# Performance work log

Measured on AMD Instinct MI355X. Metric: run time of the kernel, lower is better.

Reference implementation:

```python
import jax, jax.numpy as jnp
import numpy as np

B, H, W, T, D = 8, 32, 32, 4, 768
BLK = 4  # super-block of base tokens used to generate the static partition


def _build_descs():
    """Deterministic partition: 4x4 blocks of the 32x32 grid, scale = block_idx % 3."""
    d0, d1, d2 = [], [], []
    for t in range(T):
        i = 0
        for by in range(0, H, BLK):
            for bx in range(0, W, BLK):
                s = i % 3
                i += 1
                if s == 0:  # 16 base (scale-0) tokens
                    for yy in range(by, by + BLK):
                        for xx in range(bx, bx + BLK):
                            d0.append((yy, xx, t))
                elif s == 1:  # four 2x2 (scale-1) tokens
                    for yy in range(by, by + BLK, 2):
                        for xx in range(bx, bx + BLK, 2):
                            d1.append((yy, xx, t))
                else:  # one 4x4 (scale-2) token
                    d2.append((by, bx, t))
    return (jnp.asarray(np.array(d0, dtype=np.int32)),
            jnp.asarray(np.array(d1, dtype=np.int32)),
            jnp.asarray(np.array(d2, dtype=np.int32)))


def setup_inputs() -> dict:
    key = jax.random.key(0)
    ks = jax.random.split(key, 8)
    base = jax.random.normal(ks[0], (B, H, W, T, D), dtype=jnp.float32)
    desc0, desc1, desc2 = _build_descs()  # [1408,3], [336,3], [84,3] of (y, x, t)
    ws = 0.05  # keep conv outputs O(1)
    w1 = jax.random.normal(ks[1], (D, D, 2, 2), jnp.float32) * ws
    b1 = jax.random.normal(ks[2], (D,), jnp.float32) * ws
    w2a = jax.random.normal(ks[3], (D, D, 2, 2), jnp.float32) * ws
    b2a = jax.random.normal(ks[4], (D,), jnp.float32) * ws
    w2b = jax.random.normal(ks[5], (D, D, 2, 2), jnp.float32) * ws
    b2b = jax.random.normal(ks[6], (D,), jnp.float32) * ws
    return {"base_patch_embeddings": base, "desc0": desc0, "desc1": desc1,
            "desc2": desc2, "w1": w1, "b1": b1, "w2a": w2a, "b2a": b2a,
            "w2b": w2b, "b2b": b2b}


def _gather_blocks(base, desc, S):
    """Gather [B, N, S, S, D] blocks at (y, x, t) descriptors."""
    off = jnp.arange(S)
    ys = desc[:, 0][:, None, None] + off[None, :, None]  # [N,S,1]
    xs = desc[:, 1][:, None, None] + off[None, None, :]  # [N,1,S]
    ts = desc[:, 2][:, None, None]                       # [N,1,1]
    return base[:, ys, xs, ts, :]                        # [B,N,S,S,D]


def _down(x, w, b):
    """One k=2, s=2 conv over grouped blocks: [B,N,S,S,D] -> [B,N,S/2,S/2,D]."""
    Bn, N, S, _, Dd = x.shape
    x = x.reshape(Bn, N, S // 2, 2, S // 2, 2, Dd)
    return jnp.einsum('bnhiwjc,dcij->bnhwd', x, w) + b


def reference(base_patch_embeddings, desc0, desc1, desc2, w1, b1, w2a, b2a, w2b, b2b):
    base = base_patch_embeddings
    # scale 0: direct gather of base tokens
    tok0 = base[:, desc0[:, 0], desc0[:, 1], desc0[:, 2], :]          # [B,N0,D]
    # scale 1: 2x2 blocks -> one conv
    blk1 = _gather_blocks(base, desc1, 2)                             # [B,N1,2,2,D]
    tok1 = _down(blk1, w1, b1)[:, :, 0, 0, :]                         # [B,N1,D]
    # scale 2: 4x4 blocks -> two convs
    blk2 = _gather_blocks(base, desc2, 4)                             # [B,N2,4,4,D]
    tok2 = _down(_down(blk2, w2a, b2a), w2b, b2b)[:, :, 0, 0, :]      # [B,N2,D]
    tokens = jnp.concatenate([tok0, tok1, tok2], axis=1)              # [B,1828,D]
    # positions: (y, x, size_in_base, timestep)
    def _pos(desc, size):
        n = desc.shape[0]
        return jnp.concatenate([desc[:, :2],
                                jnp.full((n, 1), size, jnp.int32),
                                desc[:, 2:3]], axis=1)
    positions = jnp.concatenate([_pos(desc0, 1), _pos(desc1, 2), _pos(desc2, 4)], axis=0)
    return tokens, positions
```

## Files before the change

### kernel.cpp

```cpp
#include <hip/hip_runtime.h>
#include <cstdint>
#include <cstddef>

#define BB    8
#define HH    32
#define WW    32
#define TT    4
#define DD    768
#define N0    1408
#define N1    336
#define N2    84
#define NTOK  1828
#define TOK_FLOATS (BB*NTOK*DD)
#define KDIM  3072
#define M1    (BB*N1)
#define M2A   (BB*N2*4)
#define M2B   (BB*N2)

typedef __attribute__((ext_vector_type(8)))  short          short8v;
typedef __attribute__((ext_vector_type(8)))  unsigned short us8;
typedef __attribute__((ext_vector_type(4)))  unsigned short us4;
typedef __attribute__((ext_vector_type(16))) float          f32x16;

__device__ __forceinline__ unsigned short f2bf(float f) {
    unsigned int u = __float_as_uint(f);
    u += 0x7fffu + ((u >> 16) & 1u);
    return (unsigned short)(u >> 16);
}

__device__ __forceinline__ void cp16(const unsigned short* g, unsigned short* l) {
    __builtin_amdgcn_global_load_lds(
        (const __attribute__((address_space(1))) unsigned int*)(const void*)g,
        (__attribute__((address_space(3))) unsigned int*)(void*)l,
        16, 0, 0);
}

#define GA_BLKS 1008
#define CW_BLKS 1728
#define Z_BLKS  504
#define PREP_BLKS (GA_BLKS + CW_BLKS + Z_BLKS + 8)

__global__ __launch_bounds__(256) void prep_kernel(
    const float* __restrict__ base, const int* __restrict__ d0,
    const int* __restrict__ d1, const int* __restrict__ d2,
    const float* __restrict__ w1, const float* __restrict__ w2a,
    const float* __restrict__ w2b,
    unsigned short* __restrict__ A1, unsigned short* __restrict__ A2,
    unsigned short* __restrict__ W1, unsigned short* __restrict__ W2a,
    unsigned short* __restrict__ W2b,
    float* __restrict__ out, float* __restrict__ pos)
{
    const int blk = blockIdx.x, tid = threadIdx.x;
    if (blk < GA_BLKS) {
        int idx = blk * 256 + tid;
        int rm = idx / 48, sg = idx - rm * 48;
        int key = rm & 7;
        int p = sg / 12, cb = (sg - p * 12) * 64;
        const float* rowp;
        unsigned short* dst;
        if (rm < M1) {
            int m = rm, b = m / N1, tok = m - b * N1;
            int y = d1[tok*3] + (p>>1), x = d1[tok*3+1] + (p&1), t = d1[tok*3+2];
            rowp = base + (size_t)(((b*HH + y)*WW + x)*TT + t) * DD;
            dst  = A1 + (size_t)m * KDIM + sg * 64;
        } else {
            int m = rm - M1, b = m / (N2*4), r = m - b * (N2*4);
            int n = r >> 2, hw = r & 3, h = hw >> 1, w = hw & 1;
            int y = d2[n*3] + 2*h + (p>>1), x = d2[n*3+1] + 2*w + (p&1), t = d2[n*3+2];
            rowp = base + (size_t)(((b*HH + y)*WW + x)*TT + t) * DD;
            dst  = A2 + (size_t)m * KDIM + sg * 64;
        }
        float4 v[16];
        #pragma unroll
        for (int j = 0; j < 16; ++j) v[j] = *(const float4*)(rowp + cb + j*4);
        #pragma unroll
        for (int o = 0; o < 8; ++o) {
            int s = o ^ key;
            float4 lo = v[s*2], hi = v[s*2+1];
            us8 r8;
            r8[0]=f2bf(lo.x); r8[1]=f2bf(lo.y); r8[2]=f2bf(lo.z); r8[3]=f2bf(lo.w);
            r8[4]=f2bf(hi.x); r8[5]=f2bf(hi.y); r8[6]=f2bf(hi.z); r8[7]=f2bf(hi.w);
            *(us8*)(dst + o*8) = r8;
        }
    } else if (blk < GA_BLKS + CW_BLKS) {
        int r = blk - GA_BLKS;
        int wsel = r / 576;
        int idx  = (r - wsel * 576) * 256 + tid;
        const float* w     = wsel==0 ? w1 : (wsel==1 ? w2a : w2b);
        unsigned short* Wt = wsel==0 ? W1 : (wsel==1 ? W2a : W2b);
        int d = idx / 192, cg = idx - d * 192;
        const float* src = w + (size_t)d * KDIM + cg * 16;
        float4 v0 = ((const float4*)src)[0];
        float4 v1 = ((const float4*)src)[1];
        float4 v2 = ((const float4*)src)[2];
        float4 v3 = ((const float4*)src)[3];
        int csw = ((cg*4) & ~63) | ((((cg>>1) ^ d) & 7) << 3) | ((cg & 1) * 4);
        unsigned short* ob = Wt + (size_t)d * KDIM + csw;
        float pv[4][4] = {{v0.x,v1.x,v2.x,v3.x},{v0.y,v1.y,v2.y,v3.y},
                          {v0.z,v1.z,v2.z,v3.z},{v0.w,v1.w,v2.w,v3.w}};
        #pragma unroll
        for (int p = 0; p < 4; ++p) {
            us4 o4; o4[0]=f2bf(pv[p][0]); o4[1]=f2bf(pv[p][1]);
                    o4[2]=f2bf(pv[p][2]); o4[3]=f2bf(pv[p][3]);
            *(us4*)(ob + p*DD) = o4;
        }
    } else if (blk < GA_BLKS + CW_BLKS + Z_BLKS) {
        int g = (blk - GA_BLKS - CW_BLKS) * 256 + tid;
        int d4 = g % 192, r = g / 192;
        int tk = r % N2, b = r / N2;
        float4 z = {0.f, 0.f, 0.f, 0.f};
        *(float4*)(out + ((size_t)b*NTOK + N0 + N1 + tk)*DD + d4*4) = z;
    } else {
        int n = (blk - GA_BLKS - CW_BLKS - Z_BLKS) * 256 + tid;
        if (n >= NTOK) return;
        int y, x, t, s;
        if (n < N0)         { y = d0[n*3];         x = d0[n*3+1];         t = d0[n*3+2];       s = 1; }
        else if (n < N0+N1) { int m = n - N0;      y = d1[m*3]; x = d1[m*3+1]; t = d1[m*3+2];  s = 2; }
        else                { int m = n - N0 - N1; y = d2[m*3]; x = d2[m*3+1]; t = d2[m*3+2];  s = 4; }
        pos[n*4+0] = (float)y; pos[n*4+1] = (float)x; pos[n*4+2] = (float)s; pos[n*4+3] = (float)t;
    }
}

struct GCfg {
    const unsigned short* A;
    const unsigned short* Bw;
    const float*          bias;
    float*                outf;
    unsigned short*       outb;
    int                   M;
    int                   mode;
    int                   kbeg;
    int                   kend;
};

__global__ __launch_bounds__(256) void mfma_gemm_v4(
    GCfg c0, GCfg c1, int nper, int mblks, int ngemm,
    const float* __restrict__ base, const int* __restrict__ d0,
    float* __restrict__ out0)
{
    if ((int)blockIdx.x >= ngemm) {
        int g = ((int)blockIdx.x - ngemm) * 256 + threadIdx.x;
        int r = g / 12, q = g - r * 12;
        int b = r / N0, n = r - b * N0;
        int y = d0[n*3], x = d0[n*3+1], t = d0[n*3+2];
        const float4* src = (const float4*)(base + (size_t)(((b*HH + y)*WW + x)*TT + t) * DD + q*64);
        float4*       dst = (float4*)(out0 + ((size_t)b*NTOK + n) * DD + q*64);
        float4 v[16];
        #pragma unroll
        for (int j = 0; j < 16; ++j) v[j] = src[j];
        #pragma unroll
        for (int j = 0; j < 16; ++j) dst[j] = v[j];
        return;
    }

    __shared__ unsigned short As[2][128 * 64];
    __shared__ unsigned short Bs[2][128 * 64];

    int wgid;
    {
        int nwg = ngemm, orig = blockIdx.x;
        int q = nwg >> 3, r = nwg & 7;
        int xcd = orig & 7, k = orig >> 3;
        wgid = (xcd < r ? xcd * (q + 1) : r * (q + 1) + (xcd - r) * q) + k;
    }
    GCfg cfg = c0;
    if (wgid >= nper) { cfg = c1; wgid -= nper; }
    const int nb = wgid / mblks, mb = wgid - nb * mblks;
    const int m0 = mb * 128, n0 = nb * 128;

    const int tid = threadIdx.x, lane = tid & 63;
    const int wv = tid >> 6, wr = wv >> 1, wc = wv & 1;
    const int l31 = lane & 31, l5 = lane >> 5;

    const unsigned short* agp[4];
    const unsigned short* bgp[4];
    #pragma unroll
    for (int j = 0; j < 4; ++j) {
        int ar = m0 + j*32 + (tid >> 3); if (ar >= cfg.M) ar = cfg.M - 1;
        agp[j] = cfg.A  + (size_t)ar * KDIM + cfg.kbeg + (tid & 7) * 8;
        int br = n0 + j*32 + (tid >> 3);
        bgp[j] = cfg.Bw + (size_t)br * KDIM + cfg.kbeg + (tid & 7) * 8;
    }
    const int wb = (tid >> 6) * 512;

    f32x16 acc[2][2];
    #pragma unroll
    for (int i = 0; i < 2; ++i)
        #pragma unroll
        for (int j = 0; j < 2; ++j)
            #pragma unroll
            for (int r = 0; r < 16; ++r) acc[i][j][r] = 0.f;

    auto STAGE = [&](int buf, int k0) {
        #pragma unroll
        for (int j = 0; j < 4; ++j) cp16(agp[j] + k0, &As[buf][j*2048 + wb]);
        #pragma unroll
        for (int j = 0; j < 4; ++j) cp16(bgp[j] + k0, &Bs[buf][j*2048 + wb]);
    };

    const int NIT = (cfg.kend - cfg.kbeg) >> 6;
    STAGE(0, 0);
    for (int it = 0; it < NIT; ++it) {
        const int cur = it & 1;
        if (it + 1 < NIT) {
            STAGE(cur ^ 1, (it + 1) * 64);
            asm volatile("s_waitcnt vmcnt(8)" ::: "memory");
        } else {
            asm volatile("s_waitcnt vmcnt(0)" ::: "memory");
        }
        __builtin_amdgcn_s_barrier();
        const unsigned short* Asb = As[cur];
        const unsigned short* Bsb = Bs[cur];
        #pragma unroll
        for (int ks = 0; ks < 4; ++ks) {
            const int q = ks*2 + l5;
            short8v av[2], bv[2];
            #pragma unroll
            for (int fm = 0; fm < 2; ++fm) {
                int R = wr*64 + fm*32 + l31;
                av[fm] = *(const short8v*)&Asb[R*64 + ((q ^ (R&7)))*8];
            }
            #pragma unroll
            for (int fn = 0; fn < 2; ++fn) {
                int R = wc*64 + fn*32 + l31;
                bv[fn] = *(const short8v*)&Bsb[R*64 + ((q ^ (R&7)))*8];
            }
            #pragma unroll
            for (int fm = 0; fm < 2; ++fm)
                #pragma unroll
                for (int fn = 0; fn < 2; ++fn)
                    acc[fm][fn] = __builtin_amdgcn_mfma_f32_32x32x16_bf16(
                        av[fm], bv[fn], acc[fm][fn], 0, 0, 0);
        }
        __builtin_amdgcn_s_barrier();
    }

    const int mode = cfg.mode;
    #pragma unroll
    for (int fm = 0; fm < 2; ++fm) {
        #pragma unroll
        for (int fn = 0; fn < 2; ++fn) {
            int n = n0 + wc*64 + fn*32 + l31;
            float bs = cfg.bias[n];
            #pragma unroll
            for (int reg = 0; reg < 16; ++reg) {
                int m = m0 + wr*64 + fm*32 + (reg&3) + 8*(reg>>2) + 4*l5;
                if (m >= cfg.M) continue;
                float v = acc[fm][fn][reg];
                if (mode == 0) {
                    int b = m / N1, tok = m - b*N1;
                    cfg.outf[((size_t)b*NTOK + N0 + tok)*DD + n] = v + bs;
                } else if (mode == 1) {
                    int nsw = (n & ~63) | ((((n>>3) ^ (m>>2)) & 7) << 3) | (n & 7);
                    cfg.outb[(size_t)m*DD + nsw] = f2bf(v + bs);
                } else {
                    int b = m / N2, tk = m - b*N2;
                    float add = v + (cfg.kbeg == 0 ? bs : 0.f);
                    atomicAdd(&cfg.outf[((size_t)b*NTOK + N0 + N1 + tk)*DD + n], add);
                }
            }
        }
    }
}

extern "C" void kernel_launch(void* const* d_in, const int* in_sizes, int n_in,
                              void* d_out, int out_size, void* d_ws, size_t ws_size,
                              hipStream_t stream)
{
    const float* base  = (const float*)d_in[0];
    const int*   desc0 = (const int*)  d_in[1];
    const int*   desc1 = (const int*)  d_in[2];
    const int*   desc2 = (const int*)  d_in[3];
    const float* w1    = (const float*)d_in[4];
    const float* b1    = (const float*)d_in[5];
    const float* w2a   = (const float*)d_in[6];
    const float* b2a   = (const float*)d_in[7];
    const float* w2b   = (const float*)d_in[8];
    const float* b2b   = (const float*)d_in[9];

    float* out = (float*)d_out;
    float* pos = (float*)d_out + TOK_FLOATS;
    unsigned short* ws = (unsigned short*)d_ws;

    const size_t ABF = (size_t)M1 * KDIM;
    const size_t Y1  = (size_t)M2A * DD;
    const size_t WTB = (size_t)DD * KDIM;
    unsigned short* A1  = ws;
    unsigned short* A2  = A1  + ABF;
    unsigned short* y1b = A2  + ABF;
    unsigned short* W1  = y1b + Y1;
    unsigned short* W2a = W1  + WTB;
    unsigned short* W2b = W2a + WTB;

    prep_kernel<<<PREP_BLKS, 256, 0, stream>>>(
        base, desc0, desc1, desc2, w1, w2a, w2b,
        A1, A2, W1, W2a, W2b, out, pos);

    GCfg cA = { A1, W1,  b1,  out,     nullptr, M1,  0, 0, KDIM };
    GCfg cB = { A2, W2a, b2a, nullptr, y1b,     M2A, 1, 0, KDIM };
    mfma_gemm_v4<<<252 + 528, 256, 0, stream>>>(cA, cB, 126, 21, 252, base, desc0, out);

    GCfg cC0 = { y1b, W2b, b2b, out, nullptr, M2B, 2, 0,        KDIM/2 };
    GCfg cC1 = { y1b, W2b, b2b, out, nullptr, M2B, 2, KDIM/2,   KDIM   };
    mfma_gemm_v4<<<72, 256, 0, stream>>>(cC0, cC1, 36, 6, 72, base, desc0, out);
}
```

Measured before the change: 345.4 us.

## Shrink GEMM tiles to 64x64 with 16x16 MFMA and move token copy to prep

```diff
diff --git a/kernel.cpp b/kernel.cpp
--- a/kernel.cpp
+++ b/kernel.cpp
@@ -17,10 +17,10 @@
 #define M2A   (BB*N2*4)
 #define M2B   (BB*N2)
 
-typedef __attribute__((ext_vector_type(8)))  short          short8v;
-typedef __attribute__((ext_vector_type(8)))  unsigned short us8;
-typedef __attribute__((ext_vector_type(4)))  unsigned short us4;
-typedef __attribute__((ext_vector_type(16))) float          f32x16;
+typedef __attribute__((ext_vector_type(8))) short          short8v;
+typedef __attribute__((ext_vector_type(8))) unsigned short us8;
+typedef __attribute__((ext_vector_type(4))) unsigned short us4;
+typedef __attribute__((ext_vector_type(4))) float          f32x4;
 
 __device__ __forceinline__ unsigned short f2bf(float f) {
     unsigned int u = __float_as_uint(f);
@@ -38,7 +38,8 @@
 #define GA_BLKS 1008
 #define CW_BLKS 1728
 #define Z_BLKS  504
-#define PREP_BLKS (GA_BLKS + CW_BLKS + Z_BLKS + 8)
+#define C0_BLKS 528
+#define PREP_BLKS (GA_BLKS + CW_BLKS + Z_BLKS + C0_BLKS + 8)
 
 __global__ __launch_bounds__(256) void prep_kernel(
     const float* __restrict__ base, const int* __restrict__ d0,
@@ -110,8 +111,20 @@
         int tk = r % N2, b = r / N2;
         float4 z = {0.f, 0.f, 0.f, 0.f};
         *(float4*)(out + ((size_t)b*NTOK + N0 + N1 + tk)*DD + d4*4) = z;
+    } else if (blk < GA_BLKS + CW_BLKS + Z_BLKS + C0_BLKS) {
+        int g = (blk - GA_BLKS - CW_BLKS - Z_BLKS) * 256 + tid;
+        int r = g / 12, q = g - r * 12;
+        int b = r / N0, n = r - b * N0;
+        int y = d0[n*3], x = d0[n*3+1], t = d0[n*3+2];
+        const float4* src = (const float4*)(base + (size_t)(((b*HH + y)*WW + x)*TT + t) * DD + q*64);
+        float4*       dst = (float4*)(out + ((size_t)b*NTOK + n) * DD + q*64);
+        float4 v[16];
+        #pragma unroll
+        for (int j = 0; j < 16; ++j) v[j] = src[j];
+        #pragma unroll
+        for (int j = 0; j < 16; ++j) dst[j] = v[j];
     } else {
-        int n = (blk - GA_BLKS - CW_BLKS - Z_BLKS) * 256 + tid;
+        int n = (blk - GA_BLKS - CW_BLKS - Z_BLKS - C0_BLKS) * 256 + tid;
         if (n >= NTOK) return;
         int y, x, t, s;
         if (n < N0)         { y = d0[n*3];         x = d0[n*3+1];         t = d0[n*3+2];       s = 1; }
@@ -133,32 +146,15 @@
     int                   kend;
 };
 
-__global__ __launch_bounds__(256) void mfma_gemm_v4(
-    GCfg c0, GCfg c1, int nper, int mblks, int ngemm,
-    const float* __restrict__ base, const int* __restrict__ d0,
-    float* __restrict__ out0)
+__global__ __launch_bounds__(256) void mfma_gemm_v5(
+    GCfg c0, GCfg c1, int nper, int mblks)
 {
-    if ((int)blockIdx.x >= ngemm) {
-        int g = ((int)blockIdx.x - ngemm) * 256 + threadIdx.x;
-        int r = g / 12, q = g - r * 12;
-        int b = r / N0, n = r - b * N0;
-        int y = d0[n*3], x = d0[n*3+1], t = d0[n*3+2];
-        const float4* src = (const float4*)(base + (size_t)(((b*HH + y)*WW + x)*TT + t) * DD + q*64);
-        float4*       dst = (float4*)(out0 + ((size_t)b*NTOK + n) * DD + q*64);
-        float4 v[16];
-        #pragma unroll
-        for (int j = 0; j < 16; ++j) v[j] = src[j];
-        #pragma unroll
-        for (int j = 0; j < 16; ++j) dst[j] = v[j];
-        return;
-    }
-
-    __shared__ unsigned short As[2][128 * 64];
-    __shared__ unsigned short Bs[2][128 * 64];
+    __shared__ unsigned short As[2][64 * 64];
+    __shared__ unsigned short Bs[2][64 * 64];
 
     int wgid;
     {
-        int nwg = ngemm, orig = blockIdx.x;
+        int nwg = gridDim.x, orig = blockIdx.x;
         int q = nwg >> 3, r = nwg & 7;
         int xcd = orig & 7, k = orig >> 3;
         wgid = (xcd < r ? xcd * (q + 1) : r * (q + 1) + (xcd - r) * q) + k;
@@ -166,36 +162,33 @@
     GCfg cfg = c0;
     if (wgid >= nper) { cfg = c1; wgid -= nper; }
     const int nb = wgid / mblks, mb = wgid - nb * mblks;
-    const int m0 = mb * 128, n0 = nb * 128;
+    const int m0 = mb * 64, n0 = nb * 64;
 
     const int tid = threadIdx.x, lane = tid & 63;
     const int wv = tid >> 6, wr = wv >> 1, wc = wv & 1;
-    const int l31 = lane & 31, l5 = lane >> 5;
-
-    const unsigned short* agp[4];
-    const unsigned short* bgp[4];
-    #pragma unroll
-    for (int j = 0; j < 4; ++j) {
-        int ar = m0 + j*32 + (tid >> 3); if (ar >= cfg.M) ar = cfg.M - 1;
-        agp[j] = cfg.A  + (size_t)ar * KDIM + cfg.kbeg + (tid & 7) * 8;
-        int br = n0 + j*32 + (tid >> 3);
-        bgp[j] = cfg.Bw + (size_t)br * KDIM + cfg.kbeg + (tid & 7) * 8;
-    }
+    const int lr = lane & 15, lq = lane >> 4, xr = lr & 7;
+
+    int ar0 = m0 +      (tid >> 3); if (ar0 >= cfg.M) ar0 = cfg.M - 1;
+    int ar1 = m0 + 32 + (tid >> 3); if (ar1 >= cfg.M) ar1 = cfg.M - 1;
+    const unsigned short* ag0 = cfg.A  + (size_t)ar0 * KDIM + cfg.kbeg + (tid & 7) * 8;
+    const unsigned short* ag1 = cfg.A  + (size_t)ar1 * KDIM + cfg.kbeg + (tid & 7) * 8;
+    const unsigned short* bg0 = cfg.Bw + (size_t)(n0 +      (tid >> 3)) * KDIM + cfg.kbeg + (tid & 7) * 8;
+    const unsigned short* bg1 = cfg.Bw + (size_t)(n0 + 32 + (tid >> 3)) * KDIM + cfg.kbeg + (tid & 7) * 8;
     const int wb = (tid >> 6) * 512;
 
-    f32x16 acc[2][2];
+    f32x4 acc[2][2];
     #pragma unroll
     for (int i = 0; i < 2; ++i)
         #pragma unroll
         for (int j = 0; j < 2; ++j)
             #pragma unroll
-            for (int r = 0; r < 16; ++r) acc[i][j][r] = 0.f;
+            for (int r = 0; r < 4; ++r) acc[i][j][r] = 0.f;
 
     auto STAGE = [&](int buf, int k0) {
-        #pragma unroll
-        for (int j = 0; j < 4; ++j) cp16(agp[j] + k0, &As[buf][j*2048 + wb]);
-        #pragma unroll
-        for (int j = 0; j < 4; ++j) cp16(bgp[j] + k0, &Bs[buf][j*2048 + wb]);
+        cp16(ag0 + k0, &As[buf][0*2048 + wb]);
+        cp16(ag1 + k0, &As[buf][1*2048 + wb]);
+        cp16(bg0 + k0, &Bs[buf][0*2048 + wb]);
+        cp16(bg1 + k0, &Bs[buf][1*2048 + wb]);
     };
 
     const int NIT = (cfg.kend - cfg.kbeg) >> 6;
@@ -204,7 +197,7 @@
         const int cur = it & 1;
         if (it + 1 < NIT) {
             STAGE(cur ^ 1, (it + 1) * 64);
-            asm volatile("s_waitcnt vmcnt(8)" ::: "memory");
+            asm volatile("s_waitcnt vmcnt(4)" ::: "memory");
         } else {
             asm volatile("s_waitcnt vmcnt(0)" ::: "memory");
         }
@@ -212,24 +205,23 @@
         const unsigned short* Asb = As[cur];
         const unsigned short* Bsb = Bs[cur];
         #pragma unroll
-        for (int ks = 0; ks < 4; ++ks) {
-            const int q = ks*2 + l5;
+        for (int ks = 0; ks < 2; ++ks) {
             short8v av[2], bv[2];
             #pragma unroll
             for (int fm = 0; fm < 2; ++fm) {
-                int R = wr*64 + fm*32 + l31;
-                av[fm] = *(const short8v*)&Asb[R*64 + ((q ^ (R&7)))*8];
+                int row = wr*32 + fm*16 + lr;
+                av[fm] = *(const short8v*)&Asb[row*64 + ((ks*4 + lq) ^ xr) * 8];
             }
             #pragma unroll
             for (int fn = 0; fn < 2; ++fn) {
-                int R = wc*64 + fn*32 + l31;
-                bv[fn] = *(const short8v*)&Bsb[R*64 + ((q ^ (R&7)))*8];
+                int row = wc*32 + fn*16 + lr;
+                bv[fn] = *(const short8v*)&Bsb[row*64 + ((ks*4 + lq) ^ xr) * 8];
             }
             #pragma unroll
             for (int fm = 0; fm < 2; ++fm)
                 #pragma unroll
                 for (int fn = 0; fn < 2; ++fn)
-                    acc[fm][fn] = __builtin_amdgcn_mfma_f32_32x32x16_bf16(
+                    acc[fm][fn] = __builtin_amdgcn_mfma_f32_16x16x32_bf16(
                         av[fm], bv[fn], acc[fm][fn], 0, 0, 0);
         }
         __builtin_amdgcn_s_barrier();
@@ -240,13 +232,13 @@
     for (int fm = 0; fm < 2; ++fm) {
         #pragma unroll
         for (int fn = 0; fn < 2; ++fn) {
-            int n = n0 + wc*64 + fn*32 + l31;
+            int n = n0 + wc*32 + fn*16 + lr;
             float bs = cfg.bias[n];
             #pragma unroll
-            for (int reg = 0; reg < 16; ++reg) {
-                int m = m0 + wr*64 + fm*32 + (reg&3) + 8*(reg>>2) + 4*l5;
+            for (int r = 0; r < 4; ++r) {
+                int m = m0 + wr*32 + fm*16 + lq*4 + r;
                 if (m >= cfg.M) continue;
-                float v = acc[fm][fn][reg];
+                float v = acc[fm][fn][r];
                 if (mode == 0) {
                     int b = m / N1, tok = m - b*N1;
                     cfg.outf[((size_t)b*NTOK + N0 + tok)*DD + n] = v + bs;
@@ -298,9 +290,9 @@
 
     GCfg cA = { A1, W1,  b1,  out,     nullptr, M1,  0, 0, KDIM };
     GCfg cB = { A2, W2a, b2a, nullptr, y1b,     M2A, 1, 0, KDIM };
-    mfma_gemm_v4<<<252 + 528, 256, 0, stream>>>(cA, cB, 126, 21, 252, base, desc0, out);
-
-    GCfg cC0 = { y1b, W2b, b2b, out, nullptr, M2B, 2, 0,        KDIM/2 };
-    GCfg cC1 = { y1b, W2b, b2b, out, nullptr, M2B, 2, KDIM/2,   KDIM   };
-    mfma_gemm_v4<<<72, 256, 0, stream>>>(cC0, cC1, 36, 6, 72, base, desc0, out);
-}
+    mfma_gemm_v5<<<1008, 256, 0, stream>>>(cA, cB, 504, 42);
+
+    GCfg cC0 = { y1b, W2b, b2b, out, nullptr, M2B, 2, 0,      KDIM/2 };
+    GCfg cC1 = { y1b, W2b, b2b, out, nullptr, M2B, 2, KDIM/2, KDIM   };
+    mfma_gemm_v5<<<264, 256, 0, stream>>>(cC0, cC1, 132, 11);
+}
```

After: 342.7 us. Within noise of the previous version (-0.8%).
